# Optimization experiments

Hardware: AMD Instinct MI355X
Metric: run time of the kernel (lower is better)

## Reference

```python
import jax, jax.numpy as jnp
import numpy as np

VOCAB, EMB, FILT, HID, WIN = 32000, 256, 256, 256, 3
B, S = 64, 1024
T = S - WIN + 1  # conv 'valid' output length = 1022


def setup_inputs() -> dict:
    key = jax.random.key(0)
    ks = jax.random.split(key, 12)
    inp = {}
    inp['ipts'] = jax.random.randint(ks[0], (B, S), 0, VOCAB, dtype=jnp.int64 if jax.config.jax_enable_x64 else jnp.int32)
    inp['seq_lengths'] = jax.random.randint(ks[1], (B,), 1, T + 1, dtype=jnp.int32)
    inp['h0'] = jnp.zeros((1, B, HID), jnp.float32)
    inp['c0'] = jnp.zeros((1, B, HID), jnp.float32)
    # learned params
    inp['emb'] = jax.random.normal(ks[2], (VOCAB, EMB), jnp.float32) * 0.1
    inp['emb'] = inp['emb'].at[0].set(0.0)  # padding_idx=0
    inp['conv_w'] = jax.random.normal(ks[3], (WIN, EMB, FILT), jnp.float32) * 0.05  # WIO layout
    inp['conv_b'] = jnp.zeros((FILT,), jnp.float32)
    inp['w_ih'] = jax.random.normal(ks[4], (4 * HID, FILT), jnp.float32) * 0.05  # gate order i,f,g,o
    inp['w_hh'] = jax.random.normal(ks[5], (4 * HID, HID), jnp.float32) * 0.05
    inp['b_ih'] = jnp.zeros((4 * HID,), jnp.float32)
    inp['b_hh'] = jnp.zeros((4 * HID,), jnp.float32)
    inp['lin_w'] = jax.random.normal(ks[6], (1, HID), jnp.float32) * 0.05
    inp['lin_b'] = jnp.zeros((1,), jnp.float32)
    return inp


def reference(ipts, seq_lengths, h0, c0, emb, conv_w, conv_b, w_ih, w_hh, b_ih, b_hh, lin_w, lin_b):
    # Embedding: [B,S,E]
    x = emb[ipts]
    x = jax.lax.conv_general_dilated(x, conv_w, window_strides=(1,), padding='VALID',
                                     dimension_numbers=('NWC', 'WIO', 'NWC')) + conv_b
    # time-major for the RNN: [T,B,F]
    xt = jnp.transpose(x, (1, 0, 2))

    def step(carry, x_t):
        h, c = carry
        g = x_t @ w_ih.T + h @ w_hh.T + (b_ih + b_hh)
        i, f, gg, o = jnp.split(g, 4, axis=-1)
        c = jax.nn.sigmoid(f) * c + jax.nn.sigmoid(i) * jnp.tanh(gg)
        h = jax.nn.sigmoid(o) * jnp.tanh(c)
        return (h, c), h

    _, hs = jax.lax.scan(step, (h0[0], c0[0]), xt)  # hs: [T,B,H]

    # masked mean over real lengths (dropout is identity at eval).
    t = hs.shape[0]
    mask = (jnp.arange(t)[:, None] < seq_lengths[None, :]).astype(hs.dtype)  # [T,B]
    mot = jnp.einsum('tbh,tb->bh', hs, mask) / seq_lengths[:, None].astype(hs.dtype)  # [B,H]

    out = jax.nn.sigmoid(mot @ lin_w.T + lin_b)  # [B,1]
    return out.squeeze(-1)
```

## Files before the change

kernel.cpp:

```cpp
#include <hip/hip_runtime.h>
#include <hip/hip_bf16.h>
#include <math.h>

#define TLEN 1022
#define SLEN 1024
#define NB   64
#define NE   256
#define NF   256
#define NH   256
#define NG   1024
#define TC   256

typedef _Float16 h2_t __attribute__((ext_vector_type(2)));
typedef __attribute__((ext_vector_type(8))) short bf16x8;
typedef __attribute__((ext_vector_type(4))) float f32x4;

#if defined(__has_builtin)
# if __has_builtin(__builtin_amdgcn_sdot4)
#  define HAVE_SDOT4 1
# endif
#endif
#ifndef HAVE_SDOT4
# define HAVE_SDOT4 0
#endif

__device__ __forceinline__ float sigm(float x){ return 1.f/(1.f+__expf(-x)); }
__device__ __forceinline__ float tanh_(float x){ return 1.f - 2.f/(__expf(2.f*x)+1.f); }

__device__ __forceinline__ int sdot4_acc(unsigned int a, unsigned int b, int acc){
#if HAVE_SDOT4
  return __builtin_amdgcn_sdot4((int)a, (int)b, acc, false);
#else
  int s = acc;
  #pragma unroll
  for (int e=0;e<4;++e){
    int av = (int)(signed char)((a >> (8*e)) & 0xff);
    int bv = (int)(signed char)((b >> (8*e)) & 0xff);
    s += av*bv;
  }
  return s;
#endif
}
__device__ __forceinline__ unsigned short f2bf(float x){
  __hip_bfloat16 b = __float2bfloat16(x);
  return __builtin_bit_cast(unsigned short, b);
}

__global__ __launch_bounds__(256) void k_bias(const float* __restrict__ conv_b,
                                              const float* __restrict__ w_ih,
                                              const float* __restrict__ b_ih,
                                              const float* __restrict__ b_hh,
                                              float* __restrict__ bias4){
  int g = blockIdx.x*256 + threadIdx.x;
  const float* row = w_ih + (size_t)g*NF;
  float s = b_ih[g] + b_hh[g];
  for (int f=0; f<NF; f+=4){
    float4 w4 = *(const float4*)(row+f);
    float4 c4 = *(const float4*)(conv_b+f);
    s += w4.x*c4.x + w4.y*c4.y + w4.z*c4.z + w4.w*c4.w;
  }
  bias4[g] = s;
}

__global__ __launch_bounds__(256) void k_scale(const float* __restrict__ w_hh,
                                               float* __restrict__ stepv,
                                               float* __restrict__ sws){
  int row = blockIdx.x*256 + threadIdx.x;
  const float* p = w_hh + (size_t)row*NH;
  float m = 0.f;
  for (int c=0;c<NH;c+=4){
    float4 v = *(const float4*)(p+c);
    m = fmaxf(m, fmaxf(fmaxf(fabsf(v.x),fabsf(v.y)), fmaxf(fabsf(v.z),fabsf(v.w))));
  }
  float st = fmaxf(m, 1e-20f) / 127.f;
  stepv[row] = st;
  sws[row]   = st / 127.f;
}

__global__ __launch_bounds__(256) void k_pack6(const float* __restrict__ w_hh,
                                               const float* __restrict__ stepv,
                                               uint4* __restrict__ pq6){
  int gid = blockIdx.x*256 + threadIdx.x;
  int i = gid >> 10, tid = gid & 1023;
  int w = tid >> 6, l = tid & 63, kq = w >> 2, jq = w & 3;
  unsigned int words[4];
  #pragma unroll
  for (int r=0; r<4; ++r){
    int row = jq*256 + l*4 + r;
    float st = stepv[row];
    unsigned int acc = 0;
    #pragma unroll
    for (int e=0; e<4; ++e){
      int col = kq*64 + i*4 + e;
      int q = __float2int_rn(w_hh[(size_t)row*NH + col] / st);
      q = max(-127, min(127, q));
      acc |= ((unsigned int)(unsigned char)(signed char)q) << (8*e);
    }
    words[r] = acc;
  }
  pq6[(size_t)i*1024 + tid] = make_uint4(words[0],words[1],words[2],words[3]);
}

__global__ __launch_bounds__(256) void k_cw2(const float* __restrict__ w_ih,
                                             const float* __restrict__ conv_w,
                                             unsigned short* __restrict__ cw2t){
  __shared__ float al[64][17];
  __shared__ float bl[16][64];
  const int n0  = blockIdx.x*64;
  const int m0  = blockIdx.y*64;
  const int tid = threadIdx.x;
  const int ty  = tid>>4, tx = tid&15;
  const int rr  = tid>>2, kq = (tid&3)<<2;
  float acc[4][4];
  #pragma unroll
  for (int i=0;i<4;++i){ acc[i][0]=0.f; acc[i][1]=0.f; acc[i][2]=0.f; acc[i][3]=0.f; }

  for (int k0=0; k0<256; k0+=16){
    __syncthreads();
    {
      float4 v = *(const float4*)(w_ih + (size_t)(m0+rr)*NF + k0 + kq);
      al[rr][kq+0]=v.x; al[rr][kq+1]=v.y; al[rr][kq+2]=v.z; al[rr][kq+3]=v.w;
      float4 u = *(const float4*)(conv_w + (size_t)(n0+rr)*NF + k0 + kq);
      bl[kq+0][rr]=u.x; bl[kq+1][rr]=u.y; bl[kq+2][rr]=u.z; bl[kq+3][rr]=u.w;
    }
    __syncthreads();
    #pragma unroll
    for (int kk=0; kk<16; ++kk){
      float a0=al[ty*4+0][kk], a1=al[ty*4+1][kk], a2=al[ty*4+2][kk], a3=al[ty*4+3][kk];
      float4 bv = *(const float4*)&bl[kk][tx*4];
      acc[0][0]+=a0*bv.x; acc[0][1]+=a0*bv.y; acc[0][2]+=a0*bv.z; acc[0][3]+=a0*bv.w;
      acc[1][0]+=a1*bv.x; acc[1][1]+=a1*bv.y; acc[1][2]+=a1*bv.z; acc[1][3]+=a1*bv.w;
      acc[2][0]+=a2*bv.x; acc[2][1]+=a2*bv.y; acc[2][2]+=a2*bv.z; acc[2][3]+=a2*bv.w;
      acc[3][0]+=a3*bv.x; acc[3][1]+=a3*bv.y; acc[3][2]+=a3*bv.z; acc[3][3]+=a3*bv.w;
    }
  }
  #pragma unroll
  for (int i=0;i<4;++i){
    size_t r = (size_t)m0 + ty*4 + i;
    unsigned int p0 = (unsigned int)f2bf(acc[i][0]) | ((unsigned int)f2bf(acc[i][1])<<16);
    unsigned int p1 = (unsigned int)f2bf(acc[i][2]) | ((unsigned int)f2bf(acc[i][3])<<16);
    *(uint2*)(cw2t + r*768 + n0 + tx*4) = make_uint2(p0, p1);
  }
}

__global__ __launch_bounds__(256,2) void k_fxg(const int* __restrict__ ipts,
                                               const float* __restrict__ emb,
                                               const unsigned short* __restrict__ cw2t,
                                               const float* __restrict__ bias4,
                                               unsigned short* __restrict__ xh,
                                               int t0){
  __shared__ unsigned short A_l[128][72];
  __shared__ unsigned short B_l[256][72];
  __shared__ int tokl[4][64];
  const int tid = threadIdx.x;
  const int l   = tid & 63, wv = tid >> 6;
  const int m0  = blockIdx.x * 128;
  const int n0  = blockIdx.y * 256;
  const int TL0 = m0 >> 6;
  {
    int tv = tid >> 6, b = tid & 63;
    tokl[tv][b] = ipts[b*SLEN + t0 + TL0 + tv];
  }

  f32x4 acc[4][8];
  #pragma unroll
  for (int mt=0; mt<4; ++mt)
    #pragma unroll
    for (int nt=0; nt<8; ++nt)
      acc[mt][nt] = (f32x4){0.f,0.f,0.f,0.f};

  const int wm = wv >> 1, wn = wv & 1;
  const int lr = l & 15, lk = l >> 4;

  for (int ks = 0; ks < 12; ++ks){
    const int w0 = ks >> 2;
    const int e0 = (ks & 3) << 6;
    __syncthreads();
    #pragma unroll
    for (int s = 0; s < 4; ++s){
      int seg = tid + s*256;
      int row = seg >> 3, off = seg & 7;
      int tok = tokl[(row>>6) + w0][row & 63];
      const float* src = emb + (size_t)tok*NE + e0 + off*8;
      float4 f0 = *(const float4*)src;
      float4 f1 = *(const float4*)(src+4);
      unsigned int p0 = (unsigned int)f2bf(f0.x) | ((unsigned int)f2bf(f0.y)<<16);
      unsigned int p1 = (unsigned int)f2bf(f0.z) | ((unsigned int)f2bf(f0.w)<<16);
      unsigned int p2 = (unsigned int)f2bf(f1.x) | ((unsigned int)f2bf(f1.y)<<16);
      unsigned int p3 = (unsigned int)f2bf(f1.z) | ((unsigned int)f2bf(f1.w)<<16);
      *(uint4*)&A_l[row][off*8] = make_uint4(p0,p1,p2,p3);
    }
    #pragma unroll
    for (int s = 0; s < 8; ++s){
      int seg = tid + s*256;
      int row = seg >> 3, off = seg & 7;
      uint4 v = *(const uint4*)(cw2t + (size_t)(n0+row)*768 + (ks<<6) + off*8);
      *(uint4*)&B_l[row][off*8] = v;
    }
    __syncthreads();
    #pragma unroll
    for (int kf = 0; kf < 2; ++kf){
      bf16x8 af[4], bfr[8];
      #pragma unroll
      for (int mt=0; mt<4; ++mt)
        af[mt] = *(const bf16x8*)&A_l[wm*64 + mt*16 + lr][kf*32 + lk*8];
      #pragma unroll
      for (int nt=0; nt<8; ++nt)
        bfr[nt] = *(const bf16x8*)&B_l[wn*128 + nt*16 + lr][kf*32 + lk*8];
      #pragma unroll
      for (int mt=0; mt<4; ++mt)
        #pragma unroll
        for (int nt=0; nt<8; ++nt)
          acc[mt][nt] = __builtin_amdgcn_mfma_f32_16x16x32_bf16(af[mt], bfr[nt], acc[mt][nt], 0,0,0);
    }
  }

  float bia[8];
  #pragma unroll
  for (int nt=0; nt<8; ++nt) bia[nt] = bias4[n0 + wn*128 + nt*16 + lr];
  #pragma unroll
  for (int mt=0; mt<4; ++mt){
    #pragma unroll
    for (int nt=0; nt<8; ++nt){
      #pragma unroll
      for (int r=0; r<4; ++r){
        int row = m0 + wm*64 + mt*16 + lk*4 + r;
        int col = n0 + wn*128 + nt*16 + lr;
        _Float16 hv = (_Float16)(acc[mt][nt][r] + bia[nt]);
        xh[(size_t)row*NG + col] = __builtin_bit_cast(unsigned short, hv);
      }
    }
  }
}

__global__ __attribute__((amdgpu_flat_work_group_size(1024,1024)))
__attribute__((amdgpu_waves_per_eu(4,4)))
void k_rnn6(const unsigned short* __restrict__ xh,
            const uint4* __restrict__ pq6,
            const float* __restrict__ sws,
            const float* __restrict__ h0,
            const float* __restrict__ c0,
            const int* __restrict__ seqlen,
            const float* __restrict__ lin_w,
            const float* __restrict__ lin_b,
            float* __restrict__ h_ws,
            float* __restrict__ c_ws,
            float* __restrict__ ms_ws,
            float* __restrict__ out,
            int t0, int tcount, int is_first, int is_last){
  __shared__ uint4 wlds[8][1024];
  __shared__ float part[4][1024];
  __shared__ unsigned int hq[64];
  __shared__ float red[256];
  const int tid = threadIdx.x;
  const int b   = blockIdx.x;
  const int l   = tid & 63, w = tid >> 6;
  const int kq  = w >> 2, jq = w & 3;
  const int rbase = jq*256 + l*4;

  #pragma unroll
  for (int i=0;i<8;++i) wlds[i][tid] = pq6[(size_t)i*1024 + tid];

  uint4 wreg[8];
  #pragma unroll
  for (int i=8;i<16;++i) wreg[i-8] = pq6[(size_t)i*1024 + tid];
  #pragma unroll
  for (int i=0;i<8;++i)
    asm volatile("" : "+v"(wreg[i].x), "+v"(wreg[i].y), "+v"(wreg[i].z), "+v"(wreg[i].w));

  float swr[4];
  #pragma unroll
  for (int r=0;r<4;++r) swr[r] = sws[rbase + r];

  const int L = seqlen[b];
  float creg = 0.f, msum = 0.f, hlast = 0.f;
  if (tid < 256){
    float hv;
    if (is_first){ hv = h0[(size_t)b*NH + tid]; creg = c0[(size_t)b*NH + tid]; }
    else { hv = h_ws[b*256 + tid]; creg = c_ws[b*256 + tid]; msum = ms_ws[b*256 + tid]; }
    hlast = hv;
    int q = __float2int_rn(hv * 127.f); q = max(-127, min(127, q));
    ((signed char*)hq)[tid] = (signed char)q;
  }
  __syncthreads();

  const unsigned short* xrow = xh + (size_t)b*NG + tid;

  for (int tl=0; tl<tcount; ++tl){
    unsigned short xr0=0, xr1=0, xr2=0, xr3=0;
    if (tid < 256){
      const unsigned short* xr = xrow + (size_t)tl*NB*NG;
      xr0 = xr[0]; xr1 = xr[256]; xr2 = xr[512]; xr3 = xr[768];
    }

    int pa[4] = {0,0,0,0};
    #pragma unroll
    for (int i=0;i<16;++i){
      unsigned int hw = hq[kq*16 + i];
      uint4 wv4 = (i < 8) ? wlds[i][tid] : wreg[i-8];
      pa[0] = sdot4_acc(wv4.x, hw, pa[0]);
      pa[1] = sdot4_acc(wv4.y, hw, pa[1]);
      pa[2] = sdot4_acc(wv4.z, hw, pa[2]);
      pa[3] = sdot4_acc(wv4.w, hw, pa[3]);
    }
    *(float4*)&part[kq][rbase & 1023] = make_float4(
        (float)pa[0]*swr[0], (float)pa[1]*swr[1],
        (float)pa[2]*swr[2], (float)pa[3]*swr[3]);
    __syncthreads();

    if (tid < 256){
      unsigned short xr4[4] = {xr0, xr1, xr2, xr3};
      float a[4];
      #pragma unroll
      for (int g=0; g<4; ++g){
        float s = (float)__builtin_bit_cast(_Float16, xr4[g]);
        int idx = g*256 + tid;
        #pragma unroll
        for (int k=0;k<4;++k) s += part[k][idx];
        a[g] = s;
      }
      float si = sigm(a[0]), sf = sigm(a[1]), so = sigm(a[3]);
      float tg = tanh_(a[2]);
      creg = sf*creg + si*tg;
      float h2 = so*tanh_(creg);
      if (t0 + tl < L) msum += h2;
      hlast = h2;
      int q2 = __float2int_rn(h2 * 127.f); q2 = max(-127, min(127, q2));
      ((signed char*)hq)[tid] = (signed char)q2;
    }
    __syncthreads();
  }

  if (tid < 256){
    h_ws[b*256 + tid]  = hlast;
    c_ws[b*256 + tid]  = creg;
    ms_ws[b*256 + tid] = msum;
  }

  if (is_last){
    if (tid < 256) red[tid] = (msum / (float)L) * lin_w[tid];
    __syncthreads();
    if (tid < 64){
      float s = red[tid] + red[tid+64] + red[tid+128] + red[tid+192];
      #pragma unroll
      for (int off=32; off>0; off>>=1) s += __shfl_down(s, off);
      if (tid==0) out[b] = sigm(s + lin_b[0]);
    }
  }
}

extern "C" void kernel_launch(void* const* d_in, const int* in_sizes, int n_in,
                              void* d_out, int out_size, void* d_ws, size_t ws_size,
                              hipStream_t stream){
  const int*   ipts   = (const int*)d_in[0];
  const int*   seqlen = (const int*)d_in[1];
  const float* h0     = (const float*)d_in[2];
  const float* c0     = (const float*)d_in[3];
  const float* emb    = (const float*)d_in[4];
  const float* conv_w = (const float*)d_in[5];
  const float* conv_b = (const float*)d_in[6];
  const float* w_ih   = (const float*)d_in[7];
  const float* w_hh   = (const float*)d_in[8];
  const float* b_ih   = (const float*)d_in[9];
  const float* b_hh   = (const float*)d_in[10];
  const float* lin_w  = (const float*)d_in[11];
  const float* lin_b  = (const float*)d_in[12];
  float* out = (float*)d_out;

  char* ws = (char*)d_ws;
  const size_t XH_B   = (size_t)TC*NB*NG*2;
  const size_t CW2_B  = (size_t)NG*768*2;
  const size_t PQ_B   = (size_t)16*1024*16;
  size_t off = 0;
  unsigned short* xh    = (unsigned short*)(ws + off); off += XH_B;
  unsigned short* cw2t  = (unsigned short*)(ws + off); off += CW2_B;
  uint4*          pq6   = (uint4*)(ws + off);          off += PQ_B;
  float*          stepv = (float*)(ws + off);          off += 4096;
  float*          sws   = (float*)(ws + off);          off += 4096;
  float*          bias4 = (float*)(ws + off);          off += 4096;
  float*          h_ws  = (float*)(ws + off);          off += 65536;
  float*          c_ws  = (float*)(ws + off);          off += 65536;
  float*          ms_ws = (float*)(ws + off);          off += 65536;

  k_bias <<<dim3(4),      dim3(256), 0, stream>>>(conv_b, w_ih, b_ih, b_hh, bias4);
  k_scale<<<dim3(4),      dim3(256), 0, stream>>>(w_hh, stepv, sws);
  k_pack6<<<dim3(64),     dim3(256), 0, stream>>>(w_hh, stepv, pq6);
  k_cw2  <<<dim3(12, 16), dim3(256), 0, stream>>>(w_ih, conv_w, cw2t);

  for (int t0 = 0; t0 < TLEN; t0 += TC){
    int tcount = (TLEN - t0 < TC) ? (TLEN - t0) : TC;
    int is_first = (t0 == 0), is_last = (t0 + TC >= TLEN);
    k_fxg <<<dim3(128, 4), dim3(256),  0, stream>>>(ipts, emb, cw2t, bias4, xh, t0);
    k_rnn6<<<dim3(NB),     dim3(1024), 0, stream>>>(xh, pq6, sws, h0, c0, seqlen,
                                                    lin_w, lin_b, h_ws, c_ws, ms_ws, out,
                                                    t0, tcount, is_first, is_last);
  }
}
```

Before: 1.259 ms.

## Fuse input-projection GEMM and recurrent step into one kernel with double-buffered overlap

Merges the input-projection GEMM and the LSTM recurrence into a single launch. Within that launch, 64 blocks run the recurrence over the current time chunk while the extra blocks compute the next chunk's gate inputs into a second ping-pong buffer. The chunk size is halved and the GEMM tile is reshaped for 1024-thread blocks. The LDS/register split of the recurrent weights also moves from 8/8 to 6/10. The goal is to hide the GEMM behind the serial recurrence, at the cost of more launches and more register pressure in the RNN path.

```diff
diff --git a/kernel.cpp b/kernel.cpp
--- a/kernel.cpp
+++ b/kernel.cpp
@@ -9,7 +9,7 @@
 #define NF   256
 #define NH   256
 #define NG   1024
-#define TC   256
+#define TC   128
 
 typedef _Float16 h2_t __attribute__((ext_vector_type(2)));
 typedef __attribute__((ext_vector_type(8))) short bf16x8;
@@ -143,208 +143,212 @@
   }
 }
 
-__global__ __launch_bounds__(256,2) void k_fxg(const int* __restrict__ ipts,
-                                               const float* __restrict__ emb,
-                                               const unsigned short* __restrict__ cw2t,
-                                               const float* __restrict__ bias4,
-                                               unsigned short* __restrict__ xh,
-                                               int t0){
-  __shared__ unsigned short A_l[128][72];
-  __shared__ unsigned short B_l[256][72];
-  __shared__ int tokl[4][64];
-  const int tid = threadIdx.x;
-  const int l   = tid & 63, wv = tid >> 6;
-  const int m0  = blockIdx.x * 128;
-  const int n0  = blockIdx.y * 256;
-  const int TL0 = m0 >> 6;
-  {
-    int tv = tid >> 6, b = tid & 63;
-    tokl[tv][b] = ipts[b*SLEN + t0 + TL0 + tv];
-  }
-
-  f32x4 acc[4][8];
-  #pragma unroll
-  for (int mt=0; mt<4; ++mt)
-    #pragma unroll
-    for (int nt=0; nt<8; ++nt)
-      acc[mt][nt] = (f32x4){0.f,0.f,0.f,0.f};
-
-  const int wm = wv >> 1, wn = wv & 1;
-  const int lr = l & 15, lk = l >> 4;
-
-  for (int ks = 0; ks < 12; ++ks){
-    const int w0 = ks >> 2;
-    const int e0 = (ks & 3) << 6;
-    __syncthreads();
-    #pragma unroll
-    for (int s = 0; s < 4; ++s){
-      int seg = tid + s*256;
-      int row = seg >> 3, off = seg & 7;
-      int tok = tokl[(row>>6) + w0][row & 63];
-      const float* src = emb + (size_t)tok*NE + e0 + off*8;
-      float4 f0 = *(const float4*)src;
-      float4 f1 = *(const float4*)(src+4);
-      unsigned int p0 = (unsigned int)f2bf(f0.x) | ((unsigned int)f2bf(f0.y)<<16);
-      unsigned int p1 = (unsigned int)f2bf(f0.z) | ((unsigned int)f2bf(f0.w)<<16);
-      unsigned int p2 = (unsigned int)f2bf(f1.x) | ((unsigned int)f2bf(f1.y)<<16);
-      unsigned int p3 = (unsigned int)f2bf(f1.z) | ((unsigned int)f2bf(f1.w)<<16);
-      *(uint4*)&A_l[row][off*8] = make_uint4(p0,p1,p2,p3);
-    }
-    #pragma unroll
-    for (int s = 0; s < 8; ++s){
-      int seg = tid + s*256;
-      int row = seg >> 3, off = seg & 7;
-      uint4 v = *(const uint4*)(cw2t + (size_t)(n0+row)*768 + (ks<<6) + off*8);
-      *(uint4*)&B_l[row][off*8] = v;
-    }
-    __syncthreads();
-    #pragma unroll
-    for (int kf = 0; kf < 2; ++kf){
-      bf16x8 af[4], bfr[8];
-      #pragma unroll
-      for (int mt=0; mt<4; ++mt)
-        af[mt] = *(const bf16x8*)&A_l[wm*64 + mt*16 + lr][kf*32 + lk*8];
-      #pragma unroll
-      for (int nt=0; nt<8; ++nt)
-        bfr[nt] = *(const bf16x8*)&B_l[wn*128 + nt*16 + lr][kf*32 + lk*8];
-      #pragma unroll
-      for (int mt=0; mt<4; ++mt)
-        #pragma unroll
-        for (int nt=0; nt<8; ++nt)
-          acc[mt][nt] = __builtin_amdgcn_mfma_f32_16x16x32_bf16(af[mt], bfr[nt], acc[mt][nt], 0,0,0);
-    }
-  }
-
-  float bia[8];
-  #pragma unroll
-  for (int nt=0; nt<8; ++nt) bia[nt] = bias4[n0 + wn*128 + nt*16 + lr];
-  #pragma unroll
-  for (int mt=0; mt<4; ++mt){
-    #pragma unroll
-    for (int nt=0; nt<8; ++nt){
-      #pragma unroll
-      for (int r=0; r<4; ++r){
-        int row = m0 + wm*64 + mt*16 + lk*4 + r;
-        int col = n0 + wn*128 + nt*16 + lr;
-        _Float16 hv = (_Float16)(acc[mt][nt][r] + bia[nt]);
-        xh[(size_t)row*NG + col] = __builtin_bit_cast(unsigned short, hv);
-      }
-    }
-  }
-}
-
 __global__ __attribute__((amdgpu_flat_work_group_size(1024,1024)))
 __attribute__((amdgpu_waves_per_eu(4,4)))
-void k_rnn6(const unsigned short* __restrict__ xh,
-            const uint4* __restrict__ pq6,
-            const float* __restrict__ sws,
-            const float* __restrict__ h0,
-            const float* __restrict__ c0,
+void k_step(const int* __restrict__ ipts, const float* __restrict__ emb,
+            const unsigned short* __restrict__ cw2t, const float* __restrict__ bias4,
+            const unsigned short* __restrict__ xh_r, unsigned short* __restrict__ xh_w,
+            const uint4* __restrict__ pq6, const float* __restrict__ sws,
+            const float* __restrict__ h0, const float* __restrict__ c0,
             const int* __restrict__ seqlen,
-            const float* __restrict__ lin_w,
-            const float* __restrict__ lin_b,
-            float* __restrict__ h_ws,
-            float* __restrict__ c_ws,
-            float* __restrict__ ms_ws,
+            const float* __restrict__ lin_w, const float* __restrict__ lin_b,
+            float* __restrict__ h_ws, float* __restrict__ c_ws, float* __restrict__ ms_ws,
             float* __restrict__ out,
-            int t0, int tcount, int is_first, int is_last){
-  __shared__ uint4 wlds[8][1024];
-  __shared__ float part[4][1024];
-  __shared__ unsigned int hq[64];
-  __shared__ float red[256];
-  const int tid = threadIdx.x;
-  const int b   = blockIdx.x;
-  const int l   = tid & 63, w = tid >> 6;
-  const int kq  = w >> 2, jq = w & 3;
-  const int rbase = jq*256 + l*4;
-
-  #pragma unroll
-  for (int i=0;i<8;++i) wlds[i][tid] = pq6[(size_t)i*1024 + tid];
-
-  uint4 wreg[8];
-  #pragma unroll
-  for (int i=8;i<16;++i) wreg[i-8] = pq6[(size_t)i*1024 + tid];
-  #pragma unroll
-  for (int i=0;i<8;++i)
-    asm volatile("" : "+v"(wreg[i].x), "+v"(wreg[i].y), "+v"(wreg[i].z), "+v"(wreg[i].w));
-
-  float swr[4];
-  #pragma unroll
-  for (int r=0;r<4;++r) swr[r] = sws[rbase + r];
-
-  const int L = seqlen[b];
-  float creg = 0.f, msum = 0.f, hlast = 0.f;
-  if (tid < 256){
-    float hv;
-    if (is_first){ hv = h0[(size_t)b*NH + tid]; creg = c0[(size_t)b*NH + tid]; }
-    else { hv = h_ws[b*256 + tid]; creg = c_ws[b*256 + tid]; msum = ms_ws[b*256 + tid]; }
-    hlast = hv;
-    int q = __float2int_rn(hv * 127.f); q = max(-127, min(127, q));
-    ((signed char*)hq)[tid] = (signed char)q;
-  }
-  __syncthreads();
-
-  const unsigned short* xrow = xh + (size_t)b*NG + tid;
-
-  for (int tl=0; tl<tcount; ++tl){
-    unsigned short xr0=0, xr1=0, xr2=0, xr3=0;
+            int t0r, int tcount, int is_first, int is_last,
+            int t0f, int do_rnn, int n_fxg){
+  __shared__ __align__(16) char smem[115968];
+  const int tid  = threadIdx.x;
+  const int nrnn = do_rnn ? 64 : 0;
+
+  if ((int)blockIdx.x < nrnn){
+    uint4*        wlds = (uint4*)smem;
+    float*        part = (float*)(smem + 98304);
+    unsigned int* hq   = (unsigned int*)(smem + 114688);
+    float*        red  = (float*)(smem + 114944);
+    const int b  = blockIdx.x;
+    const int l  = tid & 63, w = tid >> 6;
+    const int kq = w >> 2, jq = w & 3;
+    const int rbase = jq*256 + l*4;
+
+    #pragma unroll
+    for (int i=0;i<6;++i) wlds[i*1024 + tid] = pq6[(size_t)i*1024 + tid];
+
+    uint4 wreg[10];
+    #pragma unroll
+    for (int i=6;i<16;++i) wreg[i-6] = pq6[(size_t)i*1024 + tid];
+    #pragma unroll
+    for (int i=0;i<10;++i)
+      asm volatile("" : "+v"(wreg[i].x), "+v"(wreg[i].y), "+v"(wreg[i].z), "+v"(wreg[i].w));
+
+    float swr[4];
+    #pragma unroll
+    for (int r=0;r<4;++r) swr[r] = sws[rbase + r];
+
+    const int L = seqlen[b];
+    float creg = 0.f, msum = 0.f, hlast = 0.f;
     if (tid < 256){
-      const unsigned short* xr = xrow + (size_t)tl*NB*NG;
-      xr0 = xr[0]; xr1 = xr[256]; xr2 = xr[512]; xr3 = xr[768];
-    }
-
-    int pa[4] = {0,0,0,0};
-    #pragma unroll
-    for (int i=0;i<16;++i){
-      unsigned int hw = hq[kq*16 + i];
-      uint4 wv4 = (i < 8) ? wlds[i][tid] : wreg[i-8];
-      pa[0] = sdot4_acc(wv4.x, hw, pa[0]);
-      pa[1] = sdot4_acc(wv4.y, hw, pa[1]);
-      pa[2] = sdot4_acc(wv4.z, hw, pa[2]);
-      pa[3] = sdot4_acc(wv4.w, hw, pa[3]);
-    }
-    *(float4*)&part[kq][rbase & 1023] = make_float4(
-        (float)pa[0]*swr[0], (float)pa[1]*swr[1],
-        (float)pa[2]*swr[2], (float)pa[3]*swr[3]);
+      float hv;
+      if (is_first){ hv = h0[(size_t)b*NH + tid]; creg = c0[(size_t)b*NH + tid]; }
+      else { hv = h_ws[b*256 + tid]; creg = c_ws[b*256 + tid]; msum = ms_ws[b*256 + tid]; }
+      hlast = hv;
+      int q = __float2int_rn(hv * 127.f); q = max(-127, min(127, q));
+      ((signed char*)hq)[tid] = (signed char)q;
+    }
     __syncthreads();
 
+    const unsigned short* xrow = xh_r + (size_t)b*NG + tid;
+
+    for (int tl=0; tl<tcount; ++tl){
+      unsigned short xr0=0, xr1=0, xr2=0, xr3=0;
+      if (tid < 256){
+        const unsigned short* xr = xrow + (size_t)tl*NB*NG;
+        xr0 = xr[0]; xr1 = xr[256]; xr2 = xr[512]; xr3 = xr[768];
+      }
+
+      unsigned int hws[16];
+      #pragma unroll
+      for (int c=0;c<4;++c){
+        uint4 t = *(const uint4*)&hq[kq*16 + c*4];
+        hws[c*4+0]=t.x; hws[c*4+1]=t.y; hws[c*4+2]=t.z; hws[c*4+3]=t.w;
+      }
+
+      int pa[4] = {0,0,0,0};
+      #pragma unroll
+      for (int i=0;i<16;++i){
+        unsigned int hw = hws[i];
+        uint4 wv4 = (i < 6) ? wlds[i*1024 + tid] : wreg[i-6];
+        pa[0] = sdot4_acc(wv4.x, hw, pa[0]);
+        pa[1] = sdot4_acc(wv4.y, hw, pa[1]);
+        pa[2] = sdot4_acc(wv4.z, hw, pa[2]);
+        pa[3] = sdot4_acc(wv4.w, hw, pa[3]);
+      }
+      *(float4*)&part[kq*1024 + rbase] = make_float4(
+          (float)pa[0]*swr[0], (float)pa[1]*swr[1],
+          (float)pa[2]*swr[2], (float)pa[3]*swr[3]);
+      __syncthreads();
+
+      if (tid < 256){
+        unsigned short xr4[4] = {xr0, xr1, xr2, xr3};
+        float a[4];
+        #pragma unroll
+        for (int g=0; g<4; ++g){
+          float s = (float)__builtin_bit_cast(_Float16, xr4[g]);
+          int idx = g*256 + tid;
+          #pragma unroll
+          for (int k=0;k<4;++k) s += part[k*1024 + idx];
+          a[g] = s;
+        }
+        float si = sigm(a[0]), sf = sigm(a[1]), so = sigm(a[3]);
+        float tg = tanh_(a[2]);
+        creg = sf*creg + si*tg;
+        float h2 = so*tanh_(creg);
+        if (t0r + tl < L) msum += h2;
+        hlast = h2;
+        int q2 = __float2int_rn(h2 * 127.f); q2 = max(-127, min(127, q2));
+        ((signed char*)hq)[tid] = (signed char)q2;
+      }
+      __syncthreads();
+    }
+
     if (tid < 256){
-      unsigned short xr4[4] = {xr0, xr1, xr2, xr3};
-      float a[4];
-      #pragma unroll
-      for (int g=0; g<4; ++g){
-        float s = (float)__builtin_bit_cast(_Float16, xr4[g]);
-        int idx = g*256 + tid;
-        #pragma unroll
-        for (int k=0;k<4;++k) s += part[k][idx];
-        a[g] = s;
-      }
-      float si = sigm(a[0]), sf = sigm(a[1]), so = sigm(a[3]);
-      float tg = tanh_(a[2]);
-      creg = sf*creg + si*tg;
-      float h2 = so*tanh_(creg);
-      if (t0 + tl < L) msum += h2;
-      hlast = h2;
-      int q2 = __float2int_rn(h2 * 127.f); q2 = max(-127, min(127, q2));
-      ((signed char*)hq)[tid] = (signed char)q2;
-    }
-    __syncthreads();
-  }
-
-  if (tid < 256){
-    h_ws[b*256 + tid]  = hlast;
-    c_ws[b*256 + tid]  = creg;
-    ms_ws[b*256 + tid] = msum;
-  }
-
-  if (is_last){
-    if (tid < 256) red[tid] = (msum / (float)L) * lin_w[tid];
-    __syncthreads();
-    if (tid < 64){
-      float s = red[tid] + red[tid+64] + red[tid+128] + red[tid+192];
-      #pragma unroll
-      for (int off=32; off>0; off>>=1) s += __shfl_down(s, off);
-      if (tid==0) out[b] = sigm(s + lin_b[0]);
+      h_ws[b*256 + tid]  = hlast;
+      c_ws[b*256 + tid]  = creg;
+      ms_ws[b*256 + tid] = msum;
+    }
+
+    if (is_last){
+      if (tid < 256) red[tid] = (msum / (float)L) * lin_w[tid];
+      __syncthreads();
+      if (tid < 64){
+        float s = red[tid] + red[tid+64] + red[tid+128] + red[tid+192];
+        #pragma unroll
+        for (int off=32; off>0; off>>=1) s += __shfl_down(s, off);
+        if (tid==0) out[b] = sigm(s + lin_b[0]);
+      }
+    }
+  } else {
+    int fidx = (int)blockIdx.x - nrnn;
+    if (fidx >= n_fxg) return;
+    unsigned short* A_l  = (unsigned short*)smem;
+    unsigned short* B_l  = (unsigned short*)(smem + 18432);
+    int*            tokl = (int*)(smem + 55296);
+    const int l  = tid & 63, wv = tid >> 6;
+    const int m0 = (fidx >> 2) * 128;
+    const int n0 = (fidx & 3) * 256;
+    const int TL0 = m0 >> 6;
+
+    if (tid < 256){
+      int tv = tid >> 6, bb = tid & 63;
+      int s = t0f + TL0 + tv;
+      tokl[tid] = (s < SLEN) ? ipts[bb*SLEN + s] : 0;
+    }
+
+    f32x4 acc[2][4];
+    #pragma unroll
+    for (int mt=0; mt<2; ++mt)
+      #pragma unroll
+      for (int nt=0; nt<4; ++nt)
+        acc[mt][nt] = (f32x4){0.f,0.f,0.f,0.f};
+
+    const int wm = wv >> 2, wn = wv & 3;
+    const int lr = l & 15, lk = l >> 4;
+
+    for (int ks = 0; ks < 12; ++ks){
+      const int w0 = ks >> 2;
+      const int e0 = (ks & 3) << 6;
+      __syncthreads();
+      {
+        int row = tid >> 3, off = tid & 7;
+        int tok = tokl[((row>>6) + w0)*64 + (row & 63)];
+        const float* src = emb + (size_t)tok*NE + e0 + off*8;
+        float4 f0 = *(const float4*)src;
+        float4 f1 = *(const float4*)(src+4);
+        unsigned int p0 = (unsigned int)f2bf(f0.x) | ((unsigned int)f2bf(f0.y)<<16);
+        unsigned int p1 = (unsigned int)f2bf(f0.z) | ((unsigned int)f2bf(f0.w)<<16);
+        unsigned int p2 = (unsigned int)f2bf(f1.x) | ((unsigned int)f2bf(f1.y)<<16);
+        unsigned int p3 = (unsigned int)f2bf(f1.z) | ((unsigned int)f2bf(f1.w)<<16);
+        *(uint4*)&A_l[row*72 + off*8] = make_uint4(p0,p1,p2,p3);
+      }
+      #pragma unroll
+      for (int s2 = 0; s2 < 2; ++s2){
+        int seg = tid + s2*1024;
+        int row = seg >> 3, off = seg & 7;
+        uint4 v = *(const uint4*)(cw2t + (size_t)(n0+row)*768 + (ks<<6) + off*8);
+        *(uint4*)&B_l[row*72 + off*8] = v;
+      }
+      __syncthreads();
+      #pragma unroll
+      for (int kf = 0; kf < 2; ++kf){
+        bf16x8 af[2], bfr[4];
+        #pragma unroll
+        for (int mt=0; mt<2; ++mt)
+          af[mt] = *(const bf16x8*)&A_l[(wm*32 + mt*16 + lr)*72 + kf*32 + lk*8];
+        #pragma unroll
+        for (int nt=0; nt<4; ++nt)
+          bfr[nt] = *(const bf16x8*)&B_l[(wn*64 + nt*16 + lr)*72 + kf*32 + lk*8];
+        #pragma unroll
+        for (int mt=0; mt<2; ++mt)
+          #pragma unroll
+          for (int nt=0; nt<4; ++nt)
+            acc[mt][nt] = __builtin_amdgcn_mfma_f32_16x16x32_bf16(af[mt], bfr[nt], acc[mt][nt], 0,0,0);
+      }
+    }
+
+    float bia[4];
+    #pragma unroll
+    for (int nt=0; nt<4; ++nt) bia[nt] = bias4[n0 + wn*64 + nt*16 + lr];
+    #pragma unroll
+    for (int mt=0; mt<2; ++mt){
+      #pragma unroll
+      for (int nt=0; nt<4; ++nt){
+        #pragma unroll
+        for (int r=0; r<4; ++r){
+          int row = m0 + wm*32 + mt*16 + lk*4 + r;
+          int col = n0 + wn*64 + nt*16 + lr;
+          _Float16 hv = (_Float16)(acc[mt][nt][r] + bia[nt]);
+          xh_w[(size_t)row*NG + col] = __builtin_bit_cast(unsigned short, hv);
+        }
+      }
     }
   }
 }
@@ -372,7 +376,8 @@
   const size_t CW2_B  = (size_t)NG*768*2;
   const size_t PQ_B   = (size_t)16*1024*16;
   size_t off = 0;
-  unsigned short* xh    = (unsigned short*)(ws + off); off += XH_B;
+  unsigned short* xhA   = (unsigned short*)(ws + off); off += XH_B;
+  unsigned short* xhB   = (unsigned short*)(ws + off); off += XH_B;
   unsigned short* cw2t  = (unsigned short*)(ws + off); off += CW2_B;
   uint4*          pq6   = (uint4*)(ws + off);          off += PQ_B;
   float*          stepv = (float*)(ws + off);          off += 4096;
@@ -387,12 +392,34 @@
   k_pack6<<<dim3(64),     dim3(256), 0, stream>>>(w_hh, stepv, pq6);
   k_cw2  <<<dim3(12, 16), dim3(256), 0, stream>>>(w_ih, conv_w, cw2t);
 
-  for (int t0 = 0; t0 < TLEN; t0 += TC){
+  unsigned short* bufs[2] = {xhA, xhB};
+  const int nchunks = (TLEN + TC - 1) / TC;
+  auto nf_of = [](int tc){ return 4 * ((tc + 1) / 2); };
+
+  {
+    int tc0 = (TLEN < TC) ? TLEN : TC;
+    int nf0 = nf_of(tc0);
+    k_step<<<dim3(nf0), dim3(1024), 0, stream>>>(
+        ipts, emb, cw2t, bias4, bufs[0], bufs[0], pq6, sws, h0, c0, seqlen,
+        lin_w, lin_b, h_ws, c_ws, ms_ws, out,
+        0, 0, 0, 0, 0, 0, nf0);
+  }
+
+  for (int c = 0; c < nchunks; ++c){
+    int t0 = c*TC;
     int tcount = (TLEN - t0 < TC) ? (TLEN - t0) : TC;
-    int is_first = (t0 == 0), is_last = (t0 + TC >= TLEN);
-    k_fxg <<<dim3(128, 4), dim3(256),  0, stream>>>(ipts, emb, cw2t, bias4, xh, t0);
-    k_rnn6<<<dim3(NB),     dim3(1024), 0, stream>>>(xh, pq6, sws, h0, c0, seqlen,
-                                                    lin_w, lin_b, h_ws, c_ws, ms_ws, out,
-                                                    t0, tcount, is_first, is_last);
-  }
-}
+    int nf = 0, t0f = 0;
+    unsigned short* xw = bufs[0];
+    if (c + 1 < nchunks){
+      int t0n = (c+1)*TC;
+      int tcn = (TLEN - t0n < TC) ? (TLEN - t0n) : TC;
+      nf  = nf_of(tcn);
+      t0f = t0n;
+      xw  = bufs[(c+1) & 1];
+    }
+    k_step<<<dim3(64 + nf), dim3(1024), 0, stream>>>(
+        ipts, emb, cw2t, bias4, bufs[c & 1], xw, pq6, sws, h0, c0, seqlen,
+        lin_w, lin_b, h_ws, c_ws, ms_ws, out,
+        t0, tcount, (c==0), (c==nchunks-1), t0f, 1, nf);
+  }
+}
```

Result: faster. 1.206 ms (median of 2 runs) (-4.2%).
